# Kernel optimization log

Measured on AMD Instinct MI355X. Metric: run time of the kernel, lower is better.

## Reference

```python
import jax, jax.numpy as jnp
import numpy as np

N_NODES = 50000


def gcn_conv(x, W, b, src, dst, n):
    # PyG GCNConv: linear transform, add self-loops, symmetric normalization,
    # scatter-add aggregation from src -> dst, then bias.
    h = x @ W  # [N, out]
    loop = jnp.arange(n, dtype=src.dtype)
    s = jnp.concatenate([src, loop])
    d = jnp.concatenate([dst, loop])
    deg = jax.ops.segment_sum(jnp.ones(s.shape[0], dtype=h.dtype), d, num_segments=n)
    dinv = jnp.where(deg > 0, jax.lax.rsqrt(deg), 0.0)
    norm = dinv[s] * dinv[d]  # [E+N]
    msg = h[s] * norm[:, None]
    out = jax.ops.segment_sum(msg, d, num_segments=n)
    return out + b


def setup_inputs() -> dict:
    key = jax.random.key(0)
    ks = jax.random.split(key, 10)
    F_in, H, C = 256, 128, 128
    E, EL = 320000, 200000
    x = jax.random.normal(ks[0], (N_NODES, F_in), dtype=jnp.float32)
    edge_index = jax.random.randint(ks[1], (2, E), 0, N_NODES, dtype=jnp.int32)
    edge_label_index = jax.random.randint(ks[2], (2, EL), 0, N_NODES, dtype=jnp.int32)
    def glorot(k, shape):
        lim = np.sqrt(6.0 / (shape[0] + shape[1]))
        return jax.random.uniform(k, shape, jnp.float32, -lim, lim)
    W0 = glorot(ks[3], (F_in, H))
    b0 = jnp.zeros((H,), jnp.float32)
    W1 = glorot(ks[4], (H, H))
    b1 = jnp.zeros((H,), jnp.float32)
    W2 = glorot(ks[5], (H, C))
    b2 = jnp.zeros((C,), jnp.float32)
    return {"x": x, "edge_index": edge_index, "edge_label_index": edge_label_index,
            "W0": W0, "b0": b0, "W1": W1, "b1": b1, "W2": W2, "b2": b2}


def reference(x, edge_index, edge_label_index, W0, b0, W1, b1, W2, b2):
    src, dst = edge_index[0], edge_index[1]
    n = x.shape[0]
    # drop_edge keep_ratio == 1.0 -> all edges kept (deterministic)
    h = jax.nn.relu(gcn_conv(x, W0, b0, src, dst, n))
    h = jax.nn.relu(gcn_conv(h, W1, b1, src, dst, n))
    z = gcn_conv(h, W2, b2, src, dst, n)  # final conv, no activation
    # decode: dot product over candidate edge pairs
    eli = edge_label_index.astype(jnp.int32)
    logits = jnp.sum(z[eli[0]] * z[eli[1]], axis=-1)  # [E_label]
    return logits
```

## Files before the change

### kernel.cpp

```cpp
#include <hip/hip_runtime.h>
#include <hip/hip_bf16.h>


typedef __attribute__((ext_vector_type(8))) short short8v;
typedef __attribute__((ext_vector_type(4))) float f32x4;

__device__ inline unsigned bf16_rne(float f) {
    unsigned u = __float_as_uint(f);
    return (u + 0x7FFF + ((u >> 16) & 1)) >> 16;
}


__global__ void count_deg_kernel(const int* __restrict__ dst, int* __restrict__ deg, int E) {
    int e = blockIdx.x * blockDim.x + threadIdx.x;
    if (e < E) atomicAdd(&deg[dst[e]], 1);
}

__global__ __launch_bounds__(1024) void scan1_kernel(int* __restrict__ data,
                                                     int* __restrict__ sums, int n) {
    __shared__ int tmp[1024];
    int t = threadIdx.x;
    int idx = blockIdx.x * 1024 + t;
    int val = (idx < n) ? data[idx] : 0;
    tmp[t] = val;
    __syncthreads();
#pragma unroll
    for (int off = 1; off < 1024; off <<= 1) {
        int v = (t >= off) ? tmp[t - off] : 0;
        __syncthreads();
        tmp[t] += v;
        __syncthreads();
    }
    if (idx < n) data[idx] = tmp[t] - val;
    if (t == 1023) sums[blockIdx.x] = tmp[t];
}

__global__ void scan2_kernel(int* __restrict__ sums, int nb) {
    int lane = threadIdx.x & 63;
    int v = (lane < nb) ? sums[lane] : 0;
    int orig = v;
#pragma unroll
    for (int d = 1; d < 64; d <<= 1) {
        int t2 = __shfl_up(v, d, 64);
        if (lane >= d) v += t2;
    }
    if (lane < nb) sums[lane] = v - orig;
}

__global__ __launch_bounds__(1024) void scan3_kernel(int* __restrict__ data,
                                                     const int* __restrict__ sums, int n) {
    int idx = blockIdx.x * 1024 + threadIdx.x;
    if (idx < n && blockIdx.x > 0) data[idx] += sums[blockIdx.x];
}

__global__ void make_dinv_kernel(const int* __restrict__ off, float* __restrict__ dinv,
                                 int n, int E) {
    int v = blockIdx.x * blockDim.x + threadIdx.x;
    if (v < n) {
        int o1 = (v + 1 < n) ? off[v + 1] : E;
        float d = (float)(o1 - off[v]) + 1.0f;
        dinv[v] = 1.0f / sqrtf(d);
    }
}

__global__ void csr_fill_kernel(const int* __restrict__ src, const int* __restrict__ dst,
                                const int* __restrict__ off, int* __restrict__ fill,
                                int* __restrict__ csr_src, int E) {
    int e = blockIdx.x * blockDim.x + threadIdx.x;
    if (e >= E) return;
    int d = dst[e];
    int pos = atomicAdd(&fill[d], 1);
    csr_src[off[d] + pos] = src[e];
}


__device__ inline void split_pack_one(const float* W, short* Whp, short* Wlp,
                                      int idx, int K) {
    int k = idx >> 7, col = idx & 127;
    float f = W[idx];
    unsigned h = bf16_rne(f);
    float fh = __uint_as_float(h << 16);
    unsigned l = bf16_rne(f - fh);
    int NS = K >> 5;
    int c = col >> 4, col16 = col & 15, s = k >> 5, q = (k >> 3) & 3, j = k & 7;
    int waddr = (c * NS + s) * 512 + q * 128 + col16 * 8 + j;
    Whp[waddr] = (short)h;
    Wlp[waddr] = (short)l;
}

__global__ void split_w_all_kernel(const float* __restrict__ W0, short* __restrict__ W0h,
                                   short* __restrict__ W0l,
                                   const float* __restrict__ W1, short* __restrict__ W1h,
                                   short* __restrict__ W1l,
                                   const float* __restrict__ W2, short* __restrict__ W2h,
                                   short* __restrict__ W2l,
                                   int n0, int n12, int K0, int K12) {
    int idx = blockIdx.x * blockDim.x + threadIdx.x;
    if (idx < n0) { split_pack_one(W0, W0h, W0l, idx, K0); return; }
    idx -= n0;
    if (idx < n12) { split_pack_one(W1, W1h, W1l, idx, K12); return; }
    idx -= n12;
    if (idx < n12) { split_pack_one(W2, W2h, W2l, idx, K12); }
}


template<int K>
__global__ __launch_bounds__(256) void pack_a_kernel(const float* __restrict__ x,
                                                     short* __restrict__ Ahp,
                                                     short* __restrict__ Alp,
                                                     int M, int ntiles) {
    int gid = blockIdx.x * blockDim.x + threadIdx.x;
    const int CH = K / 8;
    if (gid >= ntiles * 16 * CH) return;
    int r  = gid & 15;
    int c8 = (gid >> 4) % CH;
    int g  = gid / (16 * CH);
    int row = g * 16 + r;
    if (row >= M) row = M - 1;
    const float* xp = x + (size_t)row * K + c8 * 8;
    float4 v0 = *reinterpret_cast<const float4*>(xp);
    float4 v1 = *reinterpret_cast<const float4*>(xp + 4);
    float f[8] = {v0.x, v0.y, v0.z, v0.w, v1.x, v1.y, v1.z, v1.w};
    short8v hv, lv;
#pragma unroll
    for (int j = 0; j < 8; ++j) {
        unsigned h = bf16_rne(f[j]);
        float fh = __uint_as_float(h << 16);
        unsigned l = bf16_rne(f[j] - fh);
        hv[j] = (short)h;
        lv[j] = (short)l;
    }
    size_t waddr = (size_t)g * 16 * K + c8 * 128 + r * 8;
    *reinterpret_cast<short8v*>(&Ahp[waddr]) = hv;
    *reinterpret_cast<short8v*>(&Alp[waddr]) = lv;
}


template<int K>
__global__ __launch_bounds__(256) void gemm_mfma_packed(const short* __restrict__ Ahp,
                                                        const short* __restrict__ Alp,
                                                        const short* __restrict__ Whp,
                                                        const short* __restrict__ Wlp,
                                                        const float* __restrict__ dinv,
                                                        float* __restrict__ out,
                                                        int M) {
    constexpr int NS = K / 32;
    const int lane = threadIdx.x & 63;
    const int w = threadIdx.x >> 6;
    const int gtile = blockIdx.x * 4 + w;
    const int row16 = gtile * 16;
    if (row16 >= M) return;

    const short* ab = Ahp + (size_t)gtile * 16 * K + lane * 8;
    const short* lb = Alp + (size_t)gtile * 16 * K + lane * 8;

    short8v ah[NS], al[NS];
#pragma unroll
    for (int s = 0; s < NS; ++s) {
        ah[s] = *reinterpret_cast<const short8v*>(ab + s * 512);
        al[s] = *reinterpret_cast<const short8v*>(lb + s * 512);
    }

    f32x4 acc[8];
#pragma unroll
    for (int c = 0; c < 8; ++c) acc[c] = (f32x4){0.f, 0.f, 0.f, 0.f};

#pragma unroll
    for (int c = 0; c < 8; ++c) {
        const short* bb = Whp + (size_t)(c * NS) * 512 + lane * 8;
        const short* cb = Wlp + (size_t)(c * NS) * 512 + lane * 8;
#pragma unroll
        for (int s = 0; s < NS; ++s) {
            short8v bh = *reinterpret_cast<const short8v*>(bb + s * 512);
            short8v bl = *reinterpret_cast<const short8v*>(cb + s * 512);
            acc[c] = __builtin_amdgcn_mfma_f32_16x16x32_bf16(ah[s], bh, acc[c], 0, 0, 0);
            acc[c] = __builtin_amdgcn_mfma_f32_16x16x32_bf16(ah[s], bl, acc[c], 0, 0, 0);
            acc[c] = __builtin_amdgcn_mfma_f32_16x16x32_bf16(al[s], bh, acc[c], 0, 0, 0);
        }
    }

#pragma unroll
    for (int r = 0; r < 4; ++r) {
        int row = row16 + (lane >> 4) * 4 + r;
        if (row < M) {
            float ds = dinv[row];
#pragma unroll
            for (int c = 0; c < 8; ++c)
                out[(size_t)row * 128 + c * 16 + (lane & 15)] = acc[c][r] * ds;
        }
    }
}


template<int PACKED>
__global__ __launch_bounds__(512) void gather_kernel(const int* __restrict__ off,
                                                     const int* __restrict__ csr_src,
                                                     const float* __restrict__ dinv,
                                                     const float* __restrict__ hp,
                                                     const float* __restrict__ bias,
                                                     float* __restrict__ outf,
                                                     short* __restrict__ Ahp,
                                                     short* __restrict__ Alp,
                                                     int n, int E, int do_relu) {
    int v = blockIdx.x * 8 + (threadIdx.x >> 6);
    int lane = threadIdx.x & 63;
    if (v >= n) return;

    int o0 = off[v];
    int o1 = (v + 1 < n) ? off[v + 1] : E;

    const float2* __restrict__ hp2 = reinterpret_cast<const float2*>(hp);
    float2 sv = hp2[(size_t)v * 64 + lane];
    float ax = sv.x, ay = sv.y;
    float bx = 0.0f, by = 0.0f;

    for (int base = o0; base < o1; base += 64) {
        int cnt = min(64, o1 - base);
        int myidx = (lane < cnt) ? csr_src[base + lane] : 0;
        int j = 0;
        for (; j + 8 <= cnt; j += 8) {
            int i0 = __shfl(myidx, j,     64);
            int i1 = __shfl(myidx, j + 1, 64);
            int i2 = __shfl(myidx, j + 2, 64);
            int i3 = __shfl(myidx, j + 3, 64);
            int i4 = __shfl(myidx, j + 4, 64);
            int i5 = __shfl(myidx, j + 5, 64);
            int i6 = __shfl(myidx, j + 6, 64);
            int i7 = __shfl(myidx, j + 7, 64);
            float2 h0 = hp2[(size_t)i0 * 64 + lane];
            float2 h1 = hp2[(size_t)i1 * 64 + lane];
            float2 h2 = hp2[(size_t)i2 * 64 + lane];
            float2 h3 = hp2[(size_t)i3 * 64 + lane];
            float2 h4 = hp2[(size_t)i4 * 64 + lane];
            float2 h5 = hp2[(size_t)i5 * 64 + lane];
            float2 h6 = hp2[(size_t)i6 * 64 + lane];
            float2 h7 = hp2[(size_t)i7 * 64 + lane];
            ax += h0.x; ay += h0.y;  bx += h1.x; by += h1.y;
            ax += h2.x; ay += h2.y;  bx += h3.x; by += h3.y;
            ax += h4.x; ay += h4.y;  bx += h5.x; by += h5.y;
            ax += h6.x; ay += h6.y;  bx += h7.x; by += h7.y;
        }
        for (; j + 4 <= cnt; j += 4) {
            int i0 = __shfl(myidx, j,     64);
            int i1 = __shfl(myidx, j + 1, 64);
            int i2 = __shfl(myidx, j + 2, 64);
            int i3 = __shfl(myidx, j + 3, 64);
            float2 h0 = hp2[(size_t)i0 * 64 + lane];
            float2 h1 = hp2[(size_t)i1 * 64 + lane];
            float2 h2 = hp2[(size_t)i2 * 64 + lane];
            float2 h3 = hp2[(size_t)i3 * 64 + lane];
            ax += h0.x; ay += h0.y;  bx += h1.x; by += h1.y;
            ax += h2.x; ay += h2.y;  bx += h3.x; by += h3.y;
        }
        for (; j < cnt; ++j) {
            int s = __shfl(myidx, j, 64);
            float2 hv = hp2[(size_t)s * 64 + lane];
            ax += hv.x; ay += hv.y;
        }
    }

    float dv = dinv[v];
    float2 bb = *reinterpret_cast<const float2*>(&bias[lane * 2]);
    float ox = dv * (ax + bx) + bb.x;
    float oy = dv * (ay + by) + bb.y;
    if (do_relu) { ox = fmaxf(ox, 0.0f); oy = fmaxf(oy, 0.0f); }

    if (PACKED) {
        unsigned h0 = bf16_rne(ox);
        unsigned l0 = bf16_rne(ox - __uint_as_float(h0 << 16));
        unsigned h1 = bf16_rne(oy);
        unsigned l1 = bf16_rne(oy - __uint_as_float(h1 << 16));
        int g = v >> 4, r = v & 15;
        int c8 = lane >> 2;
        int j0 = (2 * lane) & 7;
        size_t a = (size_t)g * 2048 + c8 * 128 + r * 8 + j0;
        *reinterpret_cast<short2*>(&Ahp[a]) = make_short2((short)h0, (short)h1);
        *reinterpret_cast<short2*>(&Alp[a]) = make_short2((short)l0, (short)l1);
    } else {
        *reinterpret_cast<float2*>(&outf[(size_t)v * 128 + lane * 2]) = make_float2(ox, oy);
    }
}


__global__ __launch_bounds__(256) void decode_kernel(const int* __restrict__ ia,
                                                     const int* __restrict__ ib,
                                                     const float* __restrict__ z,
                                                     float* __restrict__ out, int EL) {
    int gid = blockIdx.x * blockDim.x + threadIdx.x;
    int e = gid >> 5;
    int l5 = gid & 31;
    if (e >= EL) return;
    int a = ia[e], b = ib[e];
    const float4* z4 = reinterpret_cast<const float4*>(z);
    float4 za = z4[(size_t)a * 32 + l5];
    float4 zb = z4[(size_t)b * 32 + l5];
    float s = za.x * zb.x + za.y * zb.y + za.z * zb.z + za.w * zb.w;
#pragma unroll
    for (int off = 16; off > 0; off >>= 1) s += __shfl_down(s, off, 64);
    if (l5 == 0) out[e] = s;
}


extern "C" void kernel_launch(void* const* d_in, const int* in_sizes, int n_in,
                              void* d_out, int out_size, void* d_ws, size_t ws_size,
                              hipStream_t stream) {
    const float* x   = (const float*)d_in[0];
    const int*   ei  = (const int*)d_in[1];
    const int*   eli = (const int*)d_in[2];
    const float* W0  = (const float*)d_in[3];
    const float* b0  = (const float*)d_in[4];
    const float* W1  = (const float*)d_in[5];
    const float* b1  = (const float*)d_in[6];
    const float* W2  = (const float*)d_in[7];
    const float* b2  = (const float*)d_in[8];
    float* out = (float*)d_out;

    const int H    = in_sizes[4];
    const int F_in = in_sizes[3] / H;
    const int n    = in_sizes[0] / F_in;
    const int E    = in_sizes[1] / 2;
    const int EL   = in_sizes[2] / 2;

    const int* src = ei;
    const int* dst = ei + E;
    const int* la  = eli;
    const int* lb  = eli + EL;

    const int ntiles = (n + 15) / 16;

    char* ws = (char*)d_ws;
    size_t p = 0;
    auto alloc = [&](size_t bytes) { char* r = ws + p; p = (p + bytes + 255) & ~(size_t)255; return r; };
    float* dinv    = (float*)alloc((size_t)n * 4);
    int*   off     = (int*)  alloc((size_t)n * 4);
    int*   csr_src = (int*)  alloc((size_t)E * 4);
    int*   sums    = (int*)  alloc(64 * 4);
    short* W0h     = (short*)alloc((size_t)F_in * H * 2);
    short* W0l     = (short*)alloc((size_t)F_in * H * 2);
    short* W1h     = (short*)alloc((size_t)H * H * 2);
    short* W1l     = (short*)alloc((size_t)H * H * 2);
    short* W2h     = (short*)alloc((size_t)H * H * 2);
    short* W2l     = (short*)alloc((size_t)H * H * 2);
    short* pkh     = (short*)alloc((size_t)ntiles * 16 * F_in * 2);
    short* pkl     = (short*)alloc((size_t)ntiles * 16 * F_in * 2);
    float* bufA    = (float*)alloc((size_t)n * 128 * 4);
    float* bufB    = (float*)alloc((size_t)n * 128 * 4);
    int*   fill    = (int*)bufB;

    const int T = 256;
    dim3 blk(T);

    hipMemsetAsync(off, 0, (size_t)n * 4, stream);
    hipMemsetAsync(fill, 0, (size_t)n * 4, stream);
    {
        int n0 = F_in * H, n12 = H * H;
        int tot = n0 + 2 * n12;
        split_w_all_kernel<<<(tot + T - 1) / T, blk, 0, stream>>>(
            W0, W0h, W0l, W1, W1h, W1l, W2, W2h, W2l, n0, n12, F_in, H);
    }
    {
        long long tot = (long long)ntiles * 16 * (F_in / 8);
        pack_a_kernel<256><<<(int)((tot + T - 1) / T), blk, 0, stream>>>(x, pkh, pkl, n, ntiles);
    }
    count_deg_kernel<<<(E + T - 1) / T, blk, 0, stream>>>(dst, off, E);
    int nb = (n + 1023) / 1024;
    scan1_kernel<<<nb, 1024, 0, stream>>>(off, sums, n);
    scan2_kernel<<<1, 64, 0, stream>>>(sums, nb);
    scan3_kernel<<<nb, 1024, 0, stream>>>(off, sums, n);
    make_dinv_kernel<<<(n + T - 1) / T, blk, 0, stream>>>(off, dinv, n, E);
    csr_fill_kernel<<<(E + T - 1) / T, blk, 0, stream>>>(src, dst, off, fill, csr_src, E);

    const int mblocks       = (ntiles + 3) / 4;
    const int gather_blocks = (n + 7) / 8;

    gemm_mfma_packed<256><<<mblocks, blk, 0, stream>>>(pkh, pkl, W0h, W0l, dinv, bufA, n);
    gather_kernel<1><<<gather_blocks, 512, 0, stream>>>(off, csr_src, dinv, bufA, b0,
                                                        nullptr, pkh, pkl, n, E, 1);

    gemm_mfma_packed<128><<<mblocks, blk, 0, stream>>>(pkh, pkl, W1h, W1l, dinv, bufA, n);
    gather_kernel<1><<<gather_blocks, 512, 0, stream>>>(off, csr_src, dinv, bufA, b1,
                                                        nullptr, pkh, pkl, n, E, 1);

    gemm_mfma_packed<128><<<mblocks, blk, 0, stream>>>(pkh, pkl, W2h, W2l, dinv, bufA, n);
    gather_kernel<0><<<gather_blocks, 512, 0, stream>>>(off, csr_src, dinv, bufA, b2,
                                                        bufB, nullptr, nullptr, n, E, 0);

    const int dec_blocks = (int)(((long long)EL * 32 + T - 1) / T);
    decode_kernel<<<dec_blocks, blk, 0, stream>>>(la, lb, bufB, out, EL);
}
```

Measured before the change: 332.9 us.

## Fuse preamble kernels, interleave hi/lo A tiles, split GEMM columns across waves

Merges the two memsets, the weight split and the input packing into a single preamble kernel, removing several launches. The bf16 hi/lo activation buffers are interleaved per 16-row tile into one array, and the gather kernel writes that layout. The GEMM now gives each wave half of the output columns for a tile, doubling the block count and halving the per-wave accumulators, at the cost of each wave reloading the A tile. The gather kernel moves from 512 to 1024 threads per block, 16 nodes per block.

After: 331.8 us. No clear change (-0.3%).

```diff
diff --git a/kernel.cpp b/kernel.cpp
--- a/kernel.cpp
+++ b/kernel.cpp
@@ -8,69 +8,6 @@
 __device__ inline unsigned bf16_rne(float f) {
     unsigned u = __float_as_uint(f);
     return (u + 0x7FFF + ((u >> 16) & 1)) >> 16;
-}
-
-
-__global__ void count_deg_kernel(const int* __restrict__ dst, int* __restrict__ deg, int E) {
-    int e = blockIdx.x * blockDim.x + threadIdx.x;
-    if (e < E) atomicAdd(&deg[dst[e]], 1);
-}
-
-__global__ __launch_bounds__(1024) void scan1_kernel(int* __restrict__ data,
-                                                     int* __restrict__ sums, int n) {
-    __shared__ int tmp[1024];
-    int t = threadIdx.x;
-    int idx = blockIdx.x * 1024 + t;
-    int val = (idx < n) ? data[idx] : 0;
-    tmp[t] = val;
-    __syncthreads();
-#pragma unroll
-    for (int off = 1; off < 1024; off <<= 1) {
-        int v = (t >= off) ? tmp[t - off] : 0;
-        __syncthreads();
-        tmp[t] += v;
-        __syncthreads();
-    }
-    if (idx < n) data[idx] = tmp[t] - val;
-    if (t == 1023) sums[blockIdx.x] = tmp[t];
-}
-
-__global__ void scan2_kernel(int* __restrict__ sums, int nb) {
-    int lane = threadIdx.x & 63;
-    int v = (lane < nb) ? sums[lane] : 0;
-    int orig = v;
-#pragma unroll
-    for (int d = 1; d < 64; d <<= 1) {
-        int t2 = __shfl_up(v, d, 64);
-        if (lane >= d) v += t2;
-    }
-    if (lane < nb) sums[lane] = v - orig;
-}
-
-__global__ __launch_bounds__(1024) void scan3_kernel(int* __restrict__ data,
-                                                     const int* __restrict__ sums, int n) {
-    int idx = blockIdx.x * 1024 + threadIdx.x;
-    if (idx < n && blockIdx.x > 0) data[idx] += sums[blockIdx.x];
-}
-
-__global__ void make_dinv_kernel(const int* __restrict__ off, float* __restrict__ dinv,
-                                 int n, int E) {
-    int v = blockIdx.x * blockDim.x + threadIdx.x;
-    if (v < n) {
-        int o1 = (v + 1 < n) ? off[v + 1] : E;
-        float d = (float)(o1 - off[v]) + 1.0f;
-        dinv[v] = 1.0f / sqrtf(d);
-    }
-}
-
-__global__ void csr_fill_kernel(const int* __restrict__ src, const int* __restrict__ dst,
-                                const int* __restrict__ off, int* __restrict__ fill,
-                                int* __restrict__ csr_src, int E) {
-    int e = blockIdx.x * blockDim.x + threadIdx.x;
-    if (e >= E) return;
-    int d = dst[e];
-    int pos = atomicAdd(&fill[d], 1);
-    csr_src[off[d] + pos] = src[e];
 }
 
 
@@ -88,35 +25,32 @@
     Wlp[waddr] = (short)l;
 }
 
-__global__ void split_w_all_kernel(const float* __restrict__ W0, short* __restrict__ W0h,
-                                   short* __restrict__ W0l,
-                                   const float* __restrict__ W1, short* __restrict__ W1h,
-                                   short* __restrict__ W1l,
-                                   const float* __restrict__ W2, short* __restrict__ W2h,
-                                   short* __restrict__ W2l,
-                                   int n0, int n12, int K0, int K12) {
-    int idx = blockIdx.x * blockDim.x + threadIdx.x;
-    if (idx < n0) { split_pack_one(W0, W0h, W0l, idx, K0); return; }
+__global__ __launch_bounds__(256) void preamble_kernel(
+        const float* __restrict__ W0, short* __restrict__ W0h, short* __restrict__ W0l,
+        const float* __restrict__ W1, short* __restrict__ W1h, short* __restrict__ W1l,
+        const float* __restrict__ W2, short* __restrict__ W2h, short* __restrict__ W2l,
+        const float* __restrict__ x, short* __restrict__ Axp,
+        int* __restrict__ off, int* __restrict__ fill,
+        int n, int F_in, int H, int ntiles, int total) {
+    int gid = blockIdx.x * blockDim.x + threadIdx.x;
+    if (gid >= total) return;
+    int idx = gid;
+    if (idx < n) { off[idx] = 0; fill[idx] = 0; return; }
+    idx -= n;
+    int n0 = F_in * H, n12 = H * H;
+    if (idx < n0) { split_pack_one(W0, W0h, W0l, idx, F_in); return; }
     idx -= n0;
-    if (idx < n12) { split_pack_one(W1, W1h, W1l, idx, K12); return; }
+    if (idx < n12) { split_pack_one(W1, W1h, W1l, idx, H); return; }
     idx -= n12;
-    if (idx < n12) { split_pack_one(W2, W2h, W2l, idx, K12); }
-}
-
-
-template<int K>
-__global__ __launch_bounds__(256) void pack_a_kernel(const float* __restrict__ x,
-                                                     short* __restrict__ Ahp,
-                                                     short* __restrict__ Alp,
-                                                     int M, int ntiles) {
-    int gid = blockIdx.x * blockDim.x + threadIdx.x;
+    if (idx < n12) { split_pack_one(W2, W2h, W2l, idx, H); return; }
+    idx -= n12;
+    const int K = F_in;
     const int CH = K / 8;
-    if (gid >= ntiles * 16 * CH) return;
-    int r  = gid & 15;
-    int c8 = (gid >> 4) % CH;
-    int g  = gid / (16 * CH);
+    int r  = idx & 15;
+    int c8 = (idx >> 4) % CH;
+    int g  = idx / (16 * CH);
     int row = g * 16 + r;
-    if (row >= M) row = M - 1;
+    if (row >= n) row = n - 1;
     const float* xp = x + (size_t)row * K + c8 * 8;
     float4 v0 = *reinterpret_cast<const float4*>(xp);
     float4 v1 = *reinterpret_cast<const float4*>(xp + 4);
@@ -130,29 +64,93 @@
         hv[j] = (short)h;
         lv[j] = (short)l;
     }
-    size_t waddr = (size_t)g * 16 * K + c8 * 128 + r * 8;
-    *reinterpret_cast<short8v*>(&Ahp[waddr]) = hv;
-    *reinterpret_cast<short8v*>(&Alp[waddr]) = lv;
+    size_t base = (size_t)g * (16 * K * 2) + c8 * 128 + r * 8;
+    *reinterpret_cast<short8v*>(&Axp[base]) = hv;
+    *reinterpret_cast<short8v*>(&Axp[base + 16 * K]) = lv;
+}
+
+
+__global__ void count_deg_kernel(const int* __restrict__ dst, int* __restrict__ deg, int E) {
+    int e = blockIdx.x * blockDim.x + threadIdx.x;
+    if (e < E) atomicAdd(&deg[dst[e]], 1);
+}
+
+__global__ __launch_bounds__(1024) void scan1_kernel(int* __restrict__ data,
+                                                     int* __restrict__ sums, int n) {
+    __shared__ int tmp[1024];
+    int t = threadIdx.x;
+    int idx = blockIdx.x * 1024 + t;
+    int val = (idx < n) ? data[idx] : 0;
+    tmp[t] = val;
+    __syncthreads();
+#pragma unroll
+    for (int off = 1; off < 1024; off <<= 1) {
+        int v = (t >= off) ? tmp[t - off] : 0;
+        __syncthreads();
+        tmp[t] += v;
+        __syncthreads();
+    }
+    if (idx < n) data[idx] = tmp[t] - val;
+    if (t == 1023) sums[blockIdx.x] = tmp[t];
+}
+
+__global__ void scan2_kernel(int* __restrict__ sums, int nb) {
+    int lane = threadIdx.x & 63;
+    int v = (lane < nb) ? sums[lane] : 0;
+    int orig = v;
+#pragma unroll
+    for (int d = 1; d < 64; d <<= 1) {
+        int t2 = __shfl_up(v, d, 64);
+        if (lane >= d) v += t2;
+    }
+    if (lane < nb) sums[lane] = v - orig;
+}
+
+__global__ __launch_bounds__(1024) void scan3_kernel(int* __restrict__ data,
+                                                     const int* __restrict__ sums, int n) {
+    int idx = blockIdx.x * 1024 + threadIdx.x;
+    if (idx < n && blockIdx.x > 0) data[idx] += sums[blockIdx.x];
+}
+
+__global__ void make_dinv_kernel(const int* __restrict__ off, float* __restrict__ dinv,
+                                 int n, int E) {
+    int v = blockIdx.x * blockDim.x + threadIdx.x;
+    if (v < n) {
+        int o1 = (v + 1 < n) ? off[v + 1] : E;
+        float d = (float)(o1 - off[v]) + 1.0f;
+        dinv[v] = 1.0f / sqrtf(d);
+    }
+}
+
+__global__ void csr_fill_kernel(const int* __restrict__ src, const int* __restrict__ dst,
+                                const int* __restrict__ off, int* __restrict__ fill,
+                                int* __restrict__ csr_src, int E) {
+    int e = blockIdx.x * blockDim.x + threadIdx.x;
+    if (e >= E) return;
+    int d = dst[e];
+    int pos = atomicAdd(&fill[d], 1);
+    csr_src[off[d] + pos] = src[e];
 }
 
 
 template<int K>
-__global__ __launch_bounds__(256) void gemm_mfma_packed(const short* __restrict__ Ahp,
-                                                        const short* __restrict__ Alp,
+__global__ __launch_bounds__(256) void gemm_mfma_packed(const short* __restrict__ Axp,
                                                         const short* __restrict__ Whp,
                                                         const short* __restrict__ Wlp,
                                                         const float* __restrict__ dinv,
                                                         float* __restrict__ out,
                                                         int M) {
     constexpr int NS = K / 32;
+    constexpr size_t TILE = (size_t)16 * K * 2;
     const int lane = threadIdx.x & 63;
     const int w = threadIdx.x >> 6;
-    const int gtile = blockIdx.x * 4 + w;
+    const int gtile = blockIdx.x * 2 + (w >> 1);
+    const int chalf = (w & 1) * 4;
     const int row16 = gtile * 16;
     if (row16 >= M) return;
 
-    const short* ab = Ahp + (size_t)gtile * 16 * K + lane * 8;
-    const short* lb = Alp + (size_t)gtile * 16 * K + lane * 8;
+    const short* ab = Axp + (size_t)gtile * TILE + lane * 8;
+    const short* lb = ab + 16 * K;
 
     short8v ah[NS], al[NS];
 #pragma unroll
@@ -161,21 +159,22 @@
         al[s] = *reinterpret_cast<const short8v*>(lb + s * 512);
     }
 
-    f32x4 acc[8];
-#pragma unroll
-    for (int c = 0; c < 8; ++c) acc[c] = (f32x4){0.f, 0.f, 0.f, 0.f};
-
-#pragma unroll
-    for (int c = 0; c < 8; ++c) {
+    f32x4 acc[4];
+#pragma unroll
+    for (int c = 0; c < 4; ++c) acc[c] = (f32x4){0.f, 0.f, 0.f, 0.f};
+
+#pragma unroll
+    for (int c4 = 0; c4 < 4; ++c4) {
+        int c = chalf + c4;
         const short* bb = Whp + (size_t)(c * NS) * 512 + lane * 8;
         const short* cb = Wlp + (size_t)(c * NS) * 512 + lane * 8;
 #pragma unroll
         for (int s = 0; s < NS; ++s) {
             short8v bh = *reinterpret_cast<const short8v*>(bb + s * 512);
             short8v bl = *reinterpret_cast<const short8v*>(cb + s * 512);
-            acc[c] = __builtin_amdgcn_mfma_f32_16x16x32_bf16(ah[s], bh, acc[c], 0, 0, 0);
-            acc[c] = __builtin_amdgcn_mfma_f32_16x16x32_bf16(ah[s], bl, acc[c], 0, 0, 0);
-            acc[c] = __builtin_amdgcn_mfma_f32_16x16x32_bf16(al[s], bh, acc[c], 0, 0, 0);
+            acc[c4] = __builtin_amdgcn_mfma_f32_16x16x32_bf16(ah[s], bh, acc[c4], 0, 0, 0);
+            acc[c4] = __builtin_amdgcn_mfma_f32_16x16x32_bf16(ah[s], bl, acc[c4], 0, 0, 0);
+            acc[c4] = __builtin_amdgcn_mfma_f32_16x16x32_bf16(al[s], bh, acc[c4], 0, 0, 0);
         }
     }
 
@@ -185,24 +184,23 @@
         if (row < M) {
             float ds = dinv[row];
 #pragma unroll
-            for (int c = 0; c < 8; ++c)
-                out[(size_t)row * 128 + c * 16 + (lane & 15)] = acc[c][r] * ds;
+            for (int c4 = 0; c4 < 4; ++c4)
+                out[(size_t)row * 128 + (chalf + c4) * 16 + (lane & 15)] = acc[c4][r] * ds;
         }
     }
 }
 
 
 template<int PACKED>
-__global__ __launch_bounds__(512) void gather_kernel(const int* __restrict__ off,
-                                                     const int* __restrict__ csr_src,
-                                                     const float* __restrict__ dinv,
-                                                     const float* __restrict__ hp,
-                                                     const float* __restrict__ bias,
-                                                     float* __restrict__ outf,
-                                                     short* __restrict__ Ahp,
-                                                     short* __restrict__ Alp,
-                                                     int n, int E, int do_relu) {
-    int v = blockIdx.x * 8 + (threadIdx.x >> 6);
+__global__ __launch_bounds__(1024) void gather_kernel(const int* __restrict__ off,
+                                                      const int* __restrict__ csr_src,
+                                                      const float* __restrict__ dinv,
+                                                      const float* __restrict__ hp,
+                                                      const float* __restrict__ bias,
+                                                      float* __restrict__ outf,
+                                                      short* __restrict__ Axp,
+                                                      int n, int E, int do_relu) {
+    int v = blockIdx.x * 16 + (threadIdx.x >> 6);
     int lane = threadIdx.x & 63;
     if (v >= n) return;
 
@@ -271,11 +269,9 @@
         unsigned h1 = bf16_rne(oy);
         unsigned l1 = bf16_rne(oy - __uint_as_float(h1 << 16));
         int g = v >> 4, r = v & 15;
-        int c8 = lane >> 2;
-        int j0 = (2 * lane) & 7;
-        size_t a = (size_t)g * 2048 + c8 * 128 + r * 8 + j0;
-        *reinterpret_cast<short2*>(&Ahp[a]) = make_short2((short)h0, (short)h1);
-        *reinterpret_cast<short2*>(&Alp[a]) = make_short2((short)l0, (short)l1);
+        size_t a = (size_t)g * 4096 + (lane >> 2) * 128 + r * 8 + ((2 * lane) & 7);
+        *reinterpret_cast<short2*>(&Axp[a])        = make_short2((short)h0, (short)h1);
+        *reinterpret_cast<short2*>(&Axp[a + 2048]) = make_short2((short)l0, (short)l1);
     } else {
         *reinterpret_cast<float2*>(&outf[(size_t)v * 128 + lane * 2]) = make_float2(ox, oy);
     }
@@ -341,8 +337,7 @@
     short* W1l     = (short*)alloc((size_t)H * H * 2);
     short* W2h     = (short*)alloc((size_t)H * H * 2);
     short* W2l     = (short*)alloc((size_t)H * H * 2);
-    short* pkh     = (short*)alloc((size_t)ntiles * 16 * F_in * 2);
-    short* pkl     = (short*)alloc((size_t)ntiles * 16 * F_in * 2);
+    short* Axp     = (short*)alloc((size_t)ntiles * 16 * F_in * 2 * 2);
     float* bufA    = (float*)alloc((size_t)n * 128 * 4);
     float* bufB    = (float*)alloc((size_t)n * 128 * 4);
     int*   fill    = (int*)bufB;
@@ -350,17 +345,12 @@
     const int T = 256;
     dim3 blk(T);
 
-    hipMemsetAsync(off, 0, (size_t)n * 4, stream);
-    hipMemsetAsync(fill, 0, (size_t)n * 4, stream);
     {
         int n0 = F_in * H, n12 = H * H;
-        int tot = n0 + 2 * n12;
-        split_w_all_kernel<<<(tot + T - 1) / T, blk, 0, stream>>>(
-            W0, W0h, W0l, W1, W1h, W1l, W2, W2h, W2l, n0, n12, F_in, H);
-    }
-    {
-        long long tot = (long long)ntiles * 16 * (F_in / 8);
-        pack_a_kernel<256><<<(int)((tot + T - 1) / T), blk, 0, stream>>>(x, pkh, pkl, n, ntiles);
+        long long total = (long long)n + n0 + 2 * n12 + (long long)ntiles * 16 * (F_in / 8);
+        preamble_kernel<<<(int)((total + T - 1) / T), blk, 0, stream>>>(
+            W0, W0h, W0l, W1, W1h, W1l, W2, W2h, W2l, x, Axp, off, fill,
+            n, F_in, H, ntiles, (int)total);
     }
     count_deg_kernel<<<(E + T - 1) / T, blk, 0, stream>>>(dst, off, E);
     int nb = (n + 1023) / 1024;
@@ -370,20 +360,20 @@
     make_dinv_kernel<<<(n + T - 1) / T, blk, 0, stream>>>(off, dinv, n, E);
     csr_fill_kernel<<<(E + T - 1) / T, blk, 0, stream>>>(src, dst, off, fill, csr_src, E);
 
-    const int mblocks       = (ntiles + 3) / 4;
-    const int gather_blocks = (n + 7) / 8;
-
-    gemm_mfma_packed<256><<<mblocks, blk, 0, stream>>>(pkh, pkl, W0h, W0l, dinv, bufA, n);
-    gather_kernel<1><<<gather_blocks, 512, 0, stream>>>(off, csr_src, dinv, bufA, b0,
-                                                        nullptr, pkh, pkl, n, E, 1);
-
-    gemm_mfma_packed<128><<<mblocks, blk, 0, stream>>>(pkh, pkl, W1h, W1l, dinv, bufA, n);
-    gather_kernel<1><<<gather_blocks, 512, 0, stream>>>(off, csr_src, dinv, bufA, b1,
-                                                        nullptr, pkh, pkl, n, E, 1);
-
-    gemm_mfma_packed<128><<<mblocks, blk, 0, stream>>>(pkh, pkl, W2h, W2l, dinv, bufA, n);
-    gather_kernel<0><<<gather_blocks, 512, 0, stream>>>(off, csr_src, dinv, bufA, b2,
-                                                        bufB, nullptr, nullptr, n, E, 0);
+    const int mblocks       = (ntiles + 1) / 2;
+    const int gather_blocks = (n + 15) / 16;
+
+    gemm_mfma_packed<256><<<mblocks, blk, 0, stream>>>(Axp, W0h, W0l, dinv, bufA, n);
+    gather_kernel<1><<<gather_blocks, 1024, 0, stream>>>(off, csr_src, dinv, bufA, b0,
+                                                         nullptr, Axp, n, E, 1);
+
+    gemm_mfma_packed<128><<<mblocks, blk, 0, stream>>>(Axp, W1h, W1l, dinv, bufA, n);
+    gather_kernel<1><<<gather_blocks, 1024, 0, stream>>>(off, csr_src, dinv, bufA, b1,
+                                                         nullptr, Axp, n, E, 1);
+
+    gemm_mfma_packed<128><<<mblocks, blk, 0, stream>>>(Axp, W2h, W2l, dinv, bufA, n);
+    gather_kernel<0><<<gather_blocks, 1024, 0, stream>>>(off, csr_src, dinv, bufA, b2,
+                                                         bufB, nullptr, n, E, 0);
 
     const int dec_blocks = (int)(((long long)EL * 32 + T - 1) / T);
     decode_kernel<<<dec_blocks, blk, 0, stream>>>(la, lb, bufB, out, EL);
```
